# Kernel tuning notes

Hardware: AMD Instinct MI355X
Metric: run time of the kernel (lower is better)

Reference implementation:

```python
import jax, jax.numpy as jnp
import numpy as np

# scNET (vae_flag=False, cd=False, eval mode): genes x cells matrix;
# PPI graph over 3000 genes, KNN graph over 4096 cells.
N_GENES, N_CELLS = 3000, 4096          # col_dim, row_dim
INTER_R, EMBD_R = 512, 128             # gene (rows) encoder dims
INTER_C, EMBD_C = 1024, 256            # cell (cols) encoder dims
N_LAYERS = 2
KNN_E, PPI_E = 65536, 262144
SCALE_PARAM = 3.0                      # TransformerConvReducrLayer scale_param


def setup_inputs() -> dict:
    key = jax.random.key(0)
    ks = iter(jax.random.split(key, 64))
    def lin(shape):
        fan_in = shape[-2]
        return jax.random.normal(next(ks), shape, jnp.float32) / np.sqrt(fan_in)
    inp = {}
    inp["x"] = jax.random.normal(next(ks), (N_GENES, N_CELLS), jnp.float32)
    inp["knn_ei"] = jax.random.randint(next(ks), (2, KNN_E), 0, N_CELLS)
    inp["ppi_ei"] = jax.random.randint(next(ks), (2, PPI_E), 0, N_GENES)
    inp["rl_W"] = lin((N_CELLS, N_CELLS)); inp["rl_b"] = jnp.zeros((N_CELLS,), jnp.float32)
    inp["rs_Wl"] = lin((N_LAYERS, N_CELLS, N_CELLS)); inp["rs_Wr"] = lin((N_LAYERS, N_CELLS, N_CELLS))
    inp["rs_b"] = jnp.zeros((N_LAYERS, N_CELLS), jnp.float32)
    inp["cs_Wl"] = lin((N_LAYERS, N_GENES, N_GENES)); inp["cs_Wr"] = lin((N_LAYERS, N_GENES, N_GENES))
    inp["cs_b"] = jnp.zeros((N_LAYERS, N_GENES), jnp.float32)
    inp["rg_W"] = lin((N_CELLS, INTER_R)); inp["rg_b"] = jnp.zeros((INTER_R,), jnp.float32)
    for nm in ("rq", "rk", "rv", "rsk"):
        inp[nm + "_W"] = lin((INTER_R, EMBD_R)); inp[nm + "_b"] = jnp.zeros((EMBD_R,), jnp.float32)
    inp["cg_W"] = lin((N_GENES, INTER_C)); inp["cg_b"] = jnp.zeros((INTER_C,), jnp.float32)
    for nm in ("cq", "ck", "cv", "csk"):
        inp[nm + "_W"] = lin((INTER_C, EMBD_C)); inp[nm + "_b"] = jnp.zeros((EMBD_C,), jnp.float32)
    inp["d1_W"] = lin((EMBD_C, INTER_C)); inp["d1_b"] = jnp.zeros((INTER_C,), jnp.float32)
    inp["d2_W"] = lin((INTER_C, INTER_C)); inp["d2_b"] = jnp.zeros((INTER_C,), jnp.float32)
    inp["d3_W"] = lin((INTER_C, N_GENES)); inp["d3_b"] = jnp.zeros((N_GENES,), jnp.float32)
    return inp


def sage_conv(x, ei, Wl, Wr, b):
    # PyG SAGEConv (mean aggr, root weight): lin_l(mean_{j->i} x_j) + lin_r(x_i) + b
    n = x.shape[0]
    src, dst = ei[0], ei[1]
    s = jax.ops.segment_sum(x[src], dst, num_segments=n)
    cnt = jax.ops.segment_sum(jnp.ones((ei.shape[1],), x.dtype), dst, num_segments=n)
    agg = s / jnp.maximum(cnt, 1.0)[:, None]
    return agg @ Wl + x @ Wr + b


def gcn_conv(x, ei, W, b):
    # PyG GCNConv: self loops + symmetric D^-1/2 (A+I) D^-1/2 normalization
    n = x.shape[0]
    idx = jnp.arange(n)
    src = jnp.concatenate([ei[0], idx])
    dst = jnp.concatenate([ei[1], idx])
    deg = jax.ops.segment_sum(jnp.ones((src.shape[0],), x.dtype), dst, num_segments=n)
    dinv = jax.lax.rsqrt(jnp.maximum(deg, 1.0))
    h = x @ W
    msg = h[src] * (dinv[src] * dinv[dst])[:, None]
    return jax.ops.segment_sum(msg, dst, num_segments=n) + b


def transformer_conv(x, ei, Wq, bq, Wk, bk, Wv, bv, Ws, bs, scale_param):
    # PyG TransformerConv (heads=1). scale_param=None -> per-destination segment
    # softmax; otherwise scNET's globally sigmoid-normalized attention
    # (TransformerConvReducrLayer.message): global mean/std standardize -> sigmoid.
    n = x.shape[0]
    d = Wq.shape[1]
    src, dst = ei[0], ei[1]
    q = x @ Wq + bq
    k = x @ Wk + bk
    v = x @ Wv + bv
    alpha = (q[dst] * k[src]).sum(-1) / jnp.sqrt(jnp.asarray(d, x.dtype))  # [E]
    if scale_param is None:
        m = jax.ops.segment_max(alpha, dst, num_segments=n)
        e = jnp.exp(alpha - m[dst])
        z = jax.ops.segment_sum(e, dst, num_segments=n)
        alpha = e / (z[dst] + 1e-16)
    else:
        alpha = (alpha - alpha.mean()) / ((1.0 / scale_param) * jnp.std(alpha, ddof=1))
        alpha = jax.nn.sigmoid(alpha)
    out = jax.ops.segment_sum(v[src] * alpha[:, None], dst, num_segments=n)
    return out + (x @ Ws + bs)  # root skip (lin_skip)


def reference(x, knn_ei, ppi_ei, rl_W, rl_b, rs_Wl, rs_Wr, rs_b, cs_Wl, cs_Wr, cs_b,
              rg_W, rg_b, rq_W, rq_b, rk_W, rk_b, rv_W, rv_b, rsk_W, rsk_b,
              cg_W, cg_b, cq_W, cq_b, ck_W, ck_b, cv_W, cv_b, csk_W, csk_b,
              d1_W, d1_b, d2_W, d2_b, d3_W, d3_b):
    # MutaelEncoder: row linear then alternating col/row SAGE layers (dropout=id in eval)
    h = x @ rl_W + rl_b                                   # [G, C]
    for i in range(N_LAYERS):
        h = jax.nn.leaky_relu(sage_conv(h.T, knn_ei, cs_Wl[i], cs_Wr[i], cs_b[i]), 0.01).T
        h = jax.nn.leaky_relu(sage_conv(h, ppi_ei, rs_Wl[i], rs_Wr[i], rs_b[i]), 0.01)
    # rows (gene) DimEncoder: GCN -> LeakyReLU -> TransformerConv (softmax attention)
    r = jax.nn.leaky_relu(gcn_conv(h, ppi_ei, rg_W, rg_b), 0.01)
    row_embed = transformer_conv(r, ppi_ei, rq_W, rq_b, rk_W, rk_b, rv_W, rv_b, rsk_W, rsk_b, None)
    # cols (cell) DimEncoder (reducer): GCN -> LeakyReLU -> sigmoid-normalized attention
    c = jax.nn.leaky_relu(gcn_conv(h.T, knn_ei, cg_W, cg_b), 0.01)
    col_embed = transformer_conv(c, knn_ei, cq_W, cq_b, ck_W, ck_b, cv_W, cv_b, csk_W, csk_b, SCALE_PARAM)
    # FatureDecoder (cd=False): 3-layer MLP with ReLU (dropout=id in eval)
    d = jax.nn.relu(col_embed @ d1_W + d1_b)
    d = jax.nn.relu(d @ d2_W + d2_b)
    recon = d @ d3_W + d3_b                               # [C_cells, G]
    return row_embed, col_embed, recon
```

## Files before the change

### kernel.cpp

```cpp
#include <hip/hip_runtime.h>
#include <math.h>

#define N_GENES 3000
#define N_CELLS 4096
#define GPAD    3072
#define INTER_R 512
#define EMBD_R  128
#define INTER_C 1024
#define EMBD_C  256
#define KNN_E   65536
#define PPI_E   262144

typedef unsigned short u16;
typedef __bf16 bf16x8 __attribute__((ext_vector_type(8)));
typedef float f32x4 __attribute__((ext_vector_type(4)));

__device__ __forceinline__ float b2f(u16 u) {
  union { unsigned i; float f; } x; x.i = ((unsigned)u) << 16; return x.f;
}
__device__ __forceinline__ u16 f2b(float f) {
  union { float f; unsigned i; } x; x.f = f;
  unsigned r = (x.i + 0x7FFFu + ((x.i >> 16) & 1u)) >> 16;
  return (u16)r;
}

typedef const void __attribute__((address_space(1))) gvoid;
typedef void __attribute__((address_space(3))) svoid;
__device__ __forceinline__ void gload16(const void* g, void* l) {
  __builtin_amdgcn_global_load_lds((gvoid*)g, (svoid*)l, 16, 0, 0);
}

template <int OUTF32>
__global__ __launch_bounds__(256) void mgemm_k(
    const u16* __restrict__ A, int lda, const u16* __restrict__ BT, int ldb,
    const float* __restrict__ bias, void* __restrict__ Cv, int ldc,
    int M, int N, int K, int accum, int act, int nbx) {
  __shared__ u16 As[2][128 * 32];
  __shared__ u16 Bs[2][128 * 32];
  const int t = threadIdx.x;
  const int w = t >> 6, l = t & 63;
  const int wr = w >> 1, wc = w & 1;
  const int fr = l & 15, hi = l >> 4;

  int nwg = gridDim.x;
  int bid = blockIdx.x;
  int q = nwg >> 3, r = nwg & 7, xcd = bid & 7, seq = bid >> 3;
  int sid = (xcd < r ? xcd * (q + 1) : r * (q + 1) + (xcd - r) * q) + seq;
  int by = sid / nbx, bx = sid - by * nbx;
  const int row0 = by * 128, col0 = bx * 128;

  f32x4 acc[4][4];
#pragma unroll
  for (int i = 0; i < 4; i++)
#pragma unroll
    for (int j = 0; j < 4; j++) acc[i][j] = (f32x4){0.f, 0.f, 0.f, 0.f};

  const u16* Aad[2]; const u16* Bad[2];
  char* Alds[2]; char* Blds[2];
#pragma unroll
  for (int c = 0; c < 2; c++) {
    int P = (w * 2 + c) * 64 + l;
    int prow = P >> 2, pg = (P & 3) ^ (prow & 3);
    int ar = row0 + prow; ar = ar < M ? ar : M - 1;
    int br = col0 + prow; br = br < N ? br : N - 1;
    Aad[c] = A + (size_t)ar * lda + pg * 8;
    Bad[c] = BT + (size_t)br * ldb + pg * 8;
    Alds[c] = (char*)&As[0][0] + (w * 2 + c) * 1024;
    Blds[c] = (char*)&Bs[0][0] + (w * 2 + c) * 1024;
  }
  const int nt = K >> 5;
  auto stage = [&](int tt, int b) {
    int ko = tt << 5;
#pragma unroll
    for (int c = 0; c < 2; c++) {
      gload16(Aad[c] + ko, Alds[c] + b * 8192);
      gload16(Bad[c] + ko, Blds[c] + b * 8192);
    }
  };
  auto compute = [&](int tt) {
    const u16* Ab = As[tt & 1];
    const u16* Bb = Bs[tt & 1];
    bf16x8 af[4], bfr[4];
#pragma unroll
    for (int mi = 0; mi < 4; mi++) {
      int row = wr * 64 + mi * 16 + fr;
      af[mi] = *(const bf16x8*)&Ab[row * 32 + ((hi ^ (row & 3)) << 3)];
    }
#pragma unroll
    for (int ni = 0; ni < 4; ni++) {
      int row = wc * 64 + ni * 16 + fr;
      bfr[ni] = *(const bf16x8*)&Bb[row * 32 + ((hi ^ (row & 3)) << 3)];
    }
    __builtin_amdgcn_s_setprio(1);
#pragma unroll
    for (int mi = 0; mi < 4; mi++)
#pragma unroll
      for (int ni = 0; ni < 4; ni++)
        acc[mi][ni] = __builtin_amdgcn_mfma_f32_16x16x32_bf16(
            af[mi], bfr[ni], acc[mi][ni], 0, 0, 0);
    __builtin_amdgcn_s_setprio(0);
  };

  stage(0, 0);
  if (nt > 1) stage(1, 1);
  for (int tt = 0; tt < nt - 1; tt++) {
    asm volatile("s_waitcnt vmcnt(4)" ::: "memory");
    __builtin_amdgcn_sched_barrier(0);
    __builtin_amdgcn_s_barrier();
    __builtin_amdgcn_sched_barrier(0);
    compute(tt);
    __builtin_amdgcn_sched_barrier(0);
    __builtin_amdgcn_s_barrier();
    __builtin_amdgcn_sched_barrier(0);
    if (tt + 2 < nt) stage(tt + 2, tt & 1);
  }
  asm volatile("s_waitcnt vmcnt(0)" ::: "memory");
  __builtin_amdgcn_sched_barrier(0);
  __builtin_amdgcn_s_barrier();
  __builtin_amdgcn_sched_barrier(0);
  compute(nt - 1);

#pragma unroll
  for (int mi = 0; mi < 4; mi++) {
    int mb = row0 + wr * 64 + mi * 16 + hi * 4;
#pragma unroll
    for (int rr2 = 0; rr2 < 4; rr2++) {
      int m = mb + rr2;
      if (m >= M) continue;
#pragma unroll
      for (int ni = 0; ni < 4; ni++) {
        int n = col0 + wc * 64 + ni * 16 + fr;
        if (n >= N) continue;
        float v = acc[mi][ni][rr2];
        if (bias) v += bias[n];
        if (OUTF32) {
          float* C = (float*)Cv;
          if (accum) v += C[(size_t)m * ldc + n];
          if (act == 1) v = v > 0.f ? v : 0.01f * v;
          else if (act == 2) v = fmaxf(v, 0.f);
          C[(size_t)m * ldc + n] = v;
        } else {
          u16* C = (u16*)Cv;
          if (accum) v += b2f(C[(size_t)m * ldc + n]);
          if (act == 1) v = v > 0.f ? v : 0.01f * v;
          else if (act == 2) v = fmaxf(v, 0.f);
          C[(size_t)m * ldc + n] = f2b(v);
        }
      }
    }
  }
}

__global__ void cvtw_k(const float* __restrict__ in, int K, int Nw,
                       u16* __restrict__ out, int ldb, int Kpad) {
  __shared__ float tile[32][33];
  int k0 = blockIdx.y * 32, n0 = blockIdx.x * 32;
  int tx = threadIdx.x & 31, ty = threadIdx.x >> 5;
  for (int i = ty; i < 32; i += 8)
    tile[i][tx] = (k0 + i < K && n0 + tx < Nw) ? in[(size_t)(k0 + i) * Nw + n0 + tx] : 0.f;
  __syncthreads();
  for (int i = ty; i < 32; i += 8) {
    int n = n0 + i, k = k0 + tx;
    if (n < Nw && k < Kpad) out[(size_t)n * ldb + k] = f2b(tile[tx][i]);
  }
}

__global__ void tpad_k(const u16* __restrict__ in, int R, int C, int lin,
                       u16* __restrict__ out, int ldout) {
  __shared__ u16 tile[32][33];
  int r0 = blockIdx.y * 32, c0 = blockIdx.x * 32;
  int tx = threadIdx.x & 31, ty = threadIdx.x >> 5;
  for (int i = ty; i < 32; i += 8)
    tile[i][tx] = (r0 + i < R && c0 + tx < C) ? in[(size_t)(r0 + i) * lin + c0 + tx] : (u16)0;
  __syncthreads();
  for (int i = ty; i < 32; i += 8) {
    int c = c0 + i, r = r0 + tx;
    if (c < C && r < ldout) out[(size_t)c * ldout + r] = tile[tx][i];
  }
}

__global__ void cvtx_k(const float* __restrict__ in, u16* __restrict__ out, int n) {
  int i = (blockIdx.x * 256 + threadIdx.x) * 4;
  if (i >= n) return;
  float4 v = *(const float4*)&in[i];
  uint2 o;
  o.x = (unsigned)f2b(v.x) | ((unsigned)f2b(v.y) << 16);
  o.y = (unsigned)f2b(v.z) | ((unsigned)f2b(v.w) << 16);
  *(uint2*)&out[i] = o;
}

__global__ void catbias_k(const float* b0, const float* b1, const float* b2,
                          const float* b3, int seg, float* out) {
  int i = blockIdx.x * 256 + threadIdx.x;
  if (i >= 4 * seg) return;
  const float* s = i < seg ? b0 : i < 2 * seg ? b1 : i < 3 * seg ? b2 : b3;
  out[i] = s[i & (seg - 1)];
}

__global__ void zero_i32(int* __restrict__ p, int n) {
  int i = blockIdx.x * 256 + threadIdx.x;
  if (i < n) p[i] = 0;
}
__global__ void count_k(const int* __restrict__ dst, int E, int* __restrict__ cnt) {
  int e = blockIdx.x * 256 + threadIdx.x;
  if (e < E) atomicAdd(&cnt[dst[e]], 1);
}
__global__ __launch_bounds__(1024) void scan_k(const int* __restrict__ cnt,
                                               int* __restrict__ rs, int N) {
  __shared__ int sd[1024];
  int t = threadIdx.x;
  int per = (N + 1023) >> 10;
  int base = t * per;
  int loc[4];
  int s = 0;
  for (int u = 0; u < per; u++) {
    int idx = base + u;
    loc[u] = s;
    int v = (idx < N) ? cnt[idx] : 0;
    s += v;
  }
  sd[t] = s;
  __syncthreads();
  for (int off = 1; off < 1024; off <<= 1) {
    int v = (t >= off) ? sd[t - off] : 0;
    __syncthreads();
    sd[t] += v;
    __syncthreads();
  }
  int prev = (t > 0) ? sd[t - 1] : 0;
  for (int u = 0; u < per; u++) {
    int idx = base + u;
    if (idx < N) rs[idx] = prev + loc[u];
  }
  if (t == 0) rs[N] = sd[1023];
}
__global__ void fill_k(const int* __restrict__ src, const int* __restrict__ dst, int E,
                       const int* __restrict__ rs, int* cursor,
                       int* __restrict__ csrc, int* __restrict__ ceid) {
  int e = blockIdx.x * 256 + threadIdx.x;
  if (e >= E) return;
  int d = dst[e];
  int p = atomicAdd(&cursor[d], 1);
  int b = rs[d] + p;
  csrc[b] = src[e];
  ceid[b] = e;
}
__global__ void dinv_k(const int* __restrict__ rs, float* __restrict__ dinv, int N) {
  int i = blockIdx.x * 256 + threadIdx.x;
  if (i < N) dinv[i] = rsqrtf((float)(rs[i + 1] - rs[i] + 1));
}

__global__ void sage_agg_k(const u16* __restrict__ X, int ld, const int* __restrict__ rs,
                           const int* __restrict__ csrc, u16* __restrict__ out,
                           int D, int Dpad) {
  int i = blockIdx.y;
  int j8 = (blockIdx.x * 256 + threadIdx.x) * 8;
  if (j8 >= Dpad) return;
  uint4 zo = {0, 0, 0, 0};
  if (j8 >= D) { *(uint4*)&out[(size_t)i * ld + j8] = zo; return; }
  int s = rs[i], e = rs[i + 1];
  float a[8] = {0, 0, 0, 0, 0, 0, 0, 0};
  for (int p = s; p < e; p++) {
    uint4 v = *(const uint4*)&X[(size_t)csrc[p] * ld + j8];
    a[0] += b2f(v.x & 0xffff); a[1] += b2f(v.x >> 16);
    a[2] += b2f(v.y & 0xffff); a[3] += b2f(v.y >> 16);
    a[4] += b2f(v.z & 0xffff); a[5] += b2f(v.z >> 16);
    a[6] += b2f(v.w & 0xffff); a[7] += b2f(v.w >> 16);
  }
  float inv = 1.f / fmaxf((float)(e - s), 1.f);
  uint4 o;
  o.x = (unsigned)f2b(a[0] * inv) | ((unsigned)f2b(a[1] * inv) << 16);
  o.y = (unsigned)f2b(a[2] * inv) | ((unsigned)f2b(a[3] * inv) << 16);
  o.z = (unsigned)f2b(a[4] * inv) | ((unsigned)f2b(a[5] * inv) << 16);
  o.w = (unsigned)f2b(a[6] * inv) | ((unsigned)f2b(a[7] * inv) << 16);
  *(uint4*)&out[(size_t)i * ld + j8] = o;
}

__global__ void gcn_agg_k(const u16* __restrict__ HW, int ld, const int* __restrict__ rs,
                          const int* __restrict__ csrc, const float* __restrict__ dinv,
                          const float* __restrict__ bias, u16* __restrict__ out, int D) {
  int i = blockIdx.y;
  int j8 = (blockIdx.x * 256 + threadIdx.x) * 8;
  if (j8 >= D) return;
  int s = rs[i], e = rs[i + 1];
  float a[8] = {0, 0, 0, 0, 0, 0, 0, 0};
  for (int p = s; p < e; p++) {
    int sr = csrc[p];
    float w = dinv[sr];
    uint4 v = *(const uint4*)&HW[(size_t)sr * ld + j8];
    a[0] += b2f(v.x & 0xffff) * w; a[1] += b2f(v.x >> 16) * w;
    a[2] += b2f(v.y & 0xffff) * w; a[3] += b2f(v.y >> 16) * w;
    a[4] += b2f(v.z & 0xffff) * w; a[5] += b2f(v.z >> 16) * w;
    a[6] += b2f(v.w & 0xffff) * w; a[7] += b2f(v.w >> 16) * w;
  }
  float di = dinv[i];
  uint4 sv = *(const uint4*)&HW[(size_t)i * ld + j8];
  float sf[8] = {b2f(sv.x & 0xffff), b2f(sv.x >> 16), b2f(sv.y & 0xffff), b2f(sv.y >> 16),
                 b2f(sv.z & 0xffff), b2f(sv.z >> 16), b2f(sv.w & 0xffff), b2f(sv.w >> 16)};
  unsigned o[4];
#pragma unroll
  for (int q = 0; q < 4; q++) {
    float v0 = di * a[2 * q] + sf[2 * q] * di * di + bias[j8 + 2 * q];
    float v1 = di * a[2 * q + 1] + sf[2 * q + 1] * di * di + bias[j8 + 2 * q + 1];
    v0 = v0 > 0.f ? v0 : 0.01f * v0;
    v1 = v1 > 0.f ? v1 : 0.01f * v1;
    o[q] = (unsigned)f2b(v0) | ((unsigned)f2b(v1) << 16);
  }
  *(uint4*)&out[(size_t)i * ld + j8] = *(uint4*)o;
}

__global__ void attn_row_k(const u16* __restrict__ QKVS, const int* __restrict__ rs,
                           const int* __restrict__ csrc, float* __restrict__ out, int N) {
  int node = blockIdx.x * 4 + (threadIdx.x >> 6);
  if (node >= N) return;
  int lane = threadIdx.x & 63;
  const u16* base = QKVS + (size_t)node * 512;
  unsigned qb = *(const unsigned*)&base[lane * 2];
  float qx = b2f(qb & 0xffff), qy = b2f(qb >> 16);
  int s = rs[node], e = rs[node + 1];
  float m = -1e30f, z = 0.f, ax = 0.f, ay = 0.f;
  const float scale = 0.08838834764831845f;
  for (int p = s; p < e; p++) {
    const u16* kb = QKVS + (size_t)csrc[p] * 512;
    unsigned kw = *(const unsigned*)&kb[128 + lane * 2];
    float part = qx * b2f(kw & 0xffff) + qy * b2f(kw >> 16);
#pragma unroll
    for (int off = 32; off; off >>= 1) part += __shfl_xor(part, off);
    float a = part * scale;
    float mn = fmaxf(m, a);
    float sc = __expf(m - mn);
    float wv = __expf(a - mn);
    z = z * sc + wv;
    unsigned vw = *(const unsigned*)&kb[256 + lane * 2];
    ax = ax * sc + wv * b2f(vw & 0xffff);
    ay = ay * sc + wv * b2f(vw >> 16);
    m = mn;
  }
  float inv = (e == s) ? 0.f : 1.f / (z + 1e-16f);
  unsigned sw = *(const unsigned*)&base[384 + lane * 2];
  out[(size_t)node * 128 + lane * 2] = ax * inv + b2f(sw & 0xffff);
  out[(size_t)node * 128 + lane * 2 + 1] = ay * inv + b2f(sw >> 16);
}

__global__ void col_alpha_k(const u16* __restrict__ QKVS, const int* __restrict__ src,
                            const int* __restrict__ dst, float* __restrict__ alpha, int E) {
  int e = blockIdx.x * 4 + (threadIdx.x >> 6);
  if (e >= E) return;
  int lane = threadIdx.x & 63;
  uint2 qb = *(const uint2*)&QKVS[(size_t)dst[e] * 1024 + lane * 4];
  uint2 kb = *(const uint2*)&QKVS[(size_t)src[e] * 1024 + 256 + lane * 4];
  float p = b2f(qb.x & 0xffff) * b2f(kb.x & 0xffff) + b2f(qb.x >> 16) * b2f(kb.x >> 16) +
            b2f(qb.y & 0xffff) * b2f(kb.y & 0xffff) + b2f(qb.y >> 16) * b2f(kb.y >> 16);
#pragma unroll
  for (int off = 32; off; off >>= 1) p += __shfl_xor(p, off);
  if (lane == 0) alpha[e] = p * 0.0625f;
}

__global__ void stats_k(const float* __restrict__ alpha, int E, double* __restrict__ st) {
  __shared__ double s1[256], s2[256];
  int t = threadIdx.x;
  double a1 = 0, a2 = 0;
  for (int i = blockIdx.x * 256 + t; i < E; i += gridDim.x * 256) {
    double a = alpha[i];
    a1 += a; a2 += a * a;
  }
  s1[t] = a1; s2[t] = a2;
  __syncthreads();
  for (int off = 128; off; off >>= 1) {
    if (t < off) { s1[t] += s1[t + off]; s2[t] += s2[t + off]; }
    __syncthreads();
  }
  if (t == 0) { atomicAdd(&st[0], s1[0]); atomicAdd(&st[1], s2[0]); }
}

__global__ void col_attn_agg_k(const u16* __restrict__ QKVS, const float* __restrict__ alpha,
                               const int* __restrict__ rs, const int* __restrict__ csrc,
                               const int* __restrict__ ceid, const double* __restrict__ st,
                               float* __restrict__ outf, u16* __restrict__ outb, int E) {
  int i = blockIdx.x;
  int j = threadIdx.x;
  double mean = st[0] / E;
  double var = (st[1] - E * mean * mean) / (double)(E - 1);
  float rstd = (float)(1.0 / sqrt(var));
  float fm = (float)mean;
  int s = rs[i], e = rs[i + 1];
  float acc = 0.f;
  for (int p = s; p < e; p++) {
    float a = alpha[ceid[p]];
    float x = 3.0f * (a - fm) * rstd;
    float sg = 1.f / (1.f + __expf(-x));
    acc += sg * b2f(QKVS[(size_t)csrc[p] * 1024 + 512 + j]);
  }
  float res = acc + b2f(QKVS[(size_t)i * 1024 + 768 + j]);
  outf[(size_t)i * 256 + j] = res;
  outb[(size_t)i * 256 + j] = f2b(res);
}

extern "C" void kernel_launch(void* const* d_in, const int* in_sizes, int n_in,
                              void* d_out, int out_size, void* d_ws, size_t ws_size,
                              hipStream_t stream) {
  const float* x      = (const float*)d_in[0];
  const int*   knn_ei = (const int*)d_in[1];
  const int*   ppi_ei = (const int*)d_in[2];
  const float* rl_W   = (const float*)d_in[3];
  const float* rl_b   = (const float*)d_in[4];
  const float* rs_Wl  = (const float*)d_in[5];
  const float* rs_Wr  = (const float*)d_in[6];
  const float* rs_b   = (const float*)d_in[7];
  const float* cs_Wl  = (const float*)d_in[8];
  const float* cs_Wr  = (const float*)d_in[9];
  const float* cs_b   = (const float*)d_in[10];
  const float* rg_W   = (const float*)d_in[11];
  const float* rg_b   = (const float*)d_in[12];
  const float* rq_W   = (const float*)d_in[13];
  const float* rq_b   = (const float*)d_in[14];
  const float* rk_W   = (const float*)d_in[15];
  const float* rk_b   = (const float*)d_in[16];
  const float* rv_W   = (const float*)d_in[17];
  const float* rv_b   = (const float*)d_in[18];
  const float* rsk_W  = (const float*)d_in[19];
  const float* rsk_b  = (const float*)d_in[20];
  const float* cg_W   = (const float*)d_in[21];
  const float* cg_b   = (const float*)d_in[22];
  const float* cq_W   = (const float*)d_in[23];
  const float* cq_b   = (const float*)d_in[24];
  const float* ck_W   = (const float*)d_in[25];
  const float* ck_b   = (const float*)d_in[26];
  const float* cv_W   = (const float*)d_in[27];
  const float* cv_b   = (const float*)d_in[28];
  const float* csk_W  = (const float*)d_in[29];
  const float* csk_b  = (const float*)d_in[30];
  const float* d1_W   = (const float*)d_in[31];
  const float* d1_b   = (const float*)d_in[32];
  const float* d2_W   = (const float*)d_in[33];
  const float* d2_b   = (const float*)d_in[34];
  const float* d3_W   = (const float*)d_in[35];
  const float* d3_b   = (const float*)d_in[36];
  float* out = (float*)d_out;

  char* ws = (char*)d_ws;
  size_t off = 0;
  auto alloc = [&](size_t bytes) -> void* {
    void* p = ws + off;
    off = (off + bytes + 255) & ~(size_t)255;
    return p;
  };
  const size_t PB = (size_t)N_CELLS * GPAD * 2;
  u16* P0 = (u16*)alloc(PB);
  u16* P1 = (u16*)alloc(PB);
  u16* P2 = (u16*)alloc(PB);
  u16* P3 = (u16*)alloc(PB);
  u16* xb  = (u16*)alloc((size_t)N_GENES * N_CELLS * 2);
  u16* BTs = (u16*)alloc((size_t)N_CELLS * N_CELLS * 2);
  u16* CEb = (u16*)alloc((size_t)N_CELLS * EMBD_C * 2);
  float* catb = (float*)alloc(1024 * 4);
  int* knn_rs  = (int*)alloc((N_CELLS + 1) * 4);
  int* knn_cnt = (int*)alloc(N_CELLS * 4);
  int* knn_cur = (int*)alloc(N_CELLS * 4);
  int* knn_src = (int*)alloc(KNN_E * 4);
  int* knn_eid = (int*)alloc(KNN_E * 4);
  int* ppi_rs  = (int*)alloc((N_GENES + 1) * 4);
  int* ppi_cnt = (int*)alloc(N_GENES * 4);
  int* ppi_cur = (int*)alloc(N_GENES * 4);
  int* ppi_src = (int*)alloc(PPI_E * 4);
  int* ppi_eid = (int*)alloc(PPI_E * 4);
  float* dinv_knn = (float*)alloc(N_CELLS * 4);
  float* dinv_ppi = (float*)alloc(N_GENES * 4);
  float* alphaB   = (float*)alloc(KNN_E * 4);
  double* stats   = (double*)alloc(2 * 8);

  auto cvtw = [&](const float* W, int K, int Nw, u16* dst, int ldb, int Kpad) {
    dim3 g((Nw + 31) / 32, (Kpad + 31) / 32);
    cvtw_k<<<g, 256, 0, stream>>>(W, K, Nw, dst, ldb, Kpad);
  };
  auto mg = [&](const u16* A, int lda, const u16* BT, int ldb, const float* bias,
                void* C, int ldc, int M, int N, int K, int accum, int act, int outf32) {
    int nbx = (N + 127) / 128, nby = (M + 127) / 128;
    dim3 g(nbx * nby);
    if (outf32)
      mgemm_k<1><<<g, 256, 0, stream>>>(A, lda, BT, ldb, bias, C, ldc, M, N, K, accum, act, nbx);
    else
      mgemm_k<0><<<g, 256, 0, stream>>>(A, lda, BT, ldb, bias, C, ldc, M, N, K, accum, act, nbx);
  };
  auto tpad = [&](const u16* in, int R, int C, int lin, u16* o, int ldout) {
    dim3 g((C + 31) / 32, (ldout + 31) / 32);
    tpad_k<<<g, 256, 0, stream>>>(in, R, C, lin, o, ldout);
  };
  auto sage = [&](const u16* X, int ld, const int* rs, const int* csrc, u16* o,
                  int nodes, int D, int Dpad) {
    dim3 g((Dpad / 8 + 255) / 256, nodes);
    sage_agg_k<<<g, 256, 0, stream>>>(X, ld, rs, csrc, o, D, Dpad);
  };
  auto gcn = [&](const u16* HW, int ld, const int* rs, const int* csrc, const float* dinv,
                 const float* bias, u16* o, int nodes, int D) {
    dim3 g((D / 8 + 255) / 256, nodes);
    gcn_agg_k<<<g, 256, 0, stream>>>(HW, ld, rs, csrc, dinv, bias, o, D);
  };

  zero_i32<<<(N_CELLS + 255) / 256, 256, 0, stream>>>(knn_cnt, N_CELLS);
  count_k<<<(KNN_E + 255) / 256, 256, 0, stream>>>(knn_ei + KNN_E, KNN_E, knn_cnt);
  scan_k<<<1, 1024, 0, stream>>>(knn_cnt, knn_rs, N_CELLS);
  zero_i32<<<(N_CELLS + 255) / 256, 256, 0, stream>>>(knn_cur, N_CELLS);
  fill_k<<<(KNN_E + 255) / 256, 256, 0, stream>>>(knn_ei, knn_ei + KNN_E, KNN_E,
                                                  knn_rs, knn_cur, knn_src, knn_eid);
  dinv_k<<<(N_CELLS + 255) / 256, 256, 0, stream>>>(knn_rs, dinv_knn, N_CELLS);
  zero_i32<<<(N_GENES + 255) / 256, 256, 0, stream>>>(ppi_cnt, N_GENES);
  count_k<<<(PPI_E + 255) / 256, 256, 0, stream>>>(ppi_ei + PPI_E, PPI_E, ppi_cnt);
  scan_k<<<1, 1024, 0, stream>>>(ppi_cnt, ppi_rs, N_GENES);
  zero_i32<<<(N_GENES + 255) / 256, 256, 0, stream>>>(ppi_cur, N_GENES);
  fill_k<<<(PPI_E + 255) / 256, 256, 0, stream>>>(ppi_ei, ppi_ei + PPI_E, PPI_E,
                                                  ppi_rs, ppi_cur, ppi_src, ppi_eid);
  dinv_k<<<(N_GENES + 255) / 256, 256, 0, stream>>>(ppi_rs, dinv_ppi, N_GENES);

  cvtx_k<<<(N_GENES * N_CELLS / 4 + 255) / 256, 256, 0, stream>>>(
      x, xb, N_GENES * N_CELLS);
  cvtw(rl_W, N_CELLS, N_CELLS, BTs, N_CELLS, N_CELLS);
  mg(xb, N_CELLS, BTs, N_CELLS, rl_b, P0, N_CELLS, N_GENES, N_CELLS, N_CELLS, 0, 0, 0);

  for (int i = 0; i < 2; i++) {
    const float* cWl = cs_Wl + (size_t)i * N_GENES * N_GENES;
    const float* cWr = cs_Wr + (size_t)i * N_GENES * N_GENES;
    const float* cb  = cs_b + (size_t)i * N_GENES;
    const float* rWl = rs_Wl + (size_t)i * N_CELLS * N_CELLS;
    const float* rWr = rs_Wr + (size_t)i * N_CELLS * N_CELLS;
    const float* rb  = rs_b + (size_t)i * N_CELLS;
    tpad(P0, N_GENES, N_CELLS, N_CELLS, P1, GPAD);
    sage(P1, GPAD, knn_rs, knn_src, P2, N_CELLS, N_GENES, GPAD);
    cvtw(cWl, N_GENES, N_GENES, BTs, GPAD, GPAD);
    mg(P2, GPAD, BTs, GPAD, cb, P3, GPAD, N_CELLS, N_GENES, GPAD, 0, 0, 0);
    cvtw(cWr, N_GENES, N_GENES, BTs, GPAD, GPAD);
    mg(P1, GPAD, BTs, GPAD, nullptr, P3, GPAD, N_CELLS, N_GENES, GPAD, 1, 1, 0);
    tpad(P3, N_CELLS, N_GENES, GPAD, P2, N_CELLS);
    sage(P2, N_CELLS, ppi_rs, ppi_src, P1, N_GENES, N_CELLS, N_CELLS);
    cvtw(rWl, N_CELLS, N_CELLS, BTs, N_CELLS, N_CELLS);
    mg(P1, N_CELLS, BTs, N_CELLS, rb, P0, N_CELLS, N_GENES, N_CELLS, N_CELLS, 0, 0, 0);
    cvtw(rWr, N_CELLS, N_CELLS, BTs, N_CELLS, N_CELLS);
    mg(P2, N_CELLS, BTs, N_CELLS, nullptr, P0, N_CELLS, N_GENES, N_CELLS, N_CELLS, 1, 1, 0);
  }

  cvtw(rg_W, N_CELLS, INTER_R, BTs, N_CELLS, N_CELLS);
  mg(P0, N_CELLS, BTs, N_CELLS, nullptr, P1, INTER_R, N_GENES, INTER_R, N_CELLS, 0, 0, 0);
  gcn(P1, INTER_R, ppi_rs, ppi_src, dinv_ppi, rg_b, P2, N_GENES, INTER_R);
  cvtw(rq_W, INTER_R, EMBD_R, BTs + (size_t)0 * EMBD_R * INTER_R, INTER_R, INTER_R);
  cvtw(rk_W, INTER_R, EMBD_R, BTs + (size_t)1 * EMBD_R * INTER_R, INTER_R, INTER_R);
  cvtw(rv_W, INTER_R, EMBD_R, BTs + (size_t)2 * EMBD_R * INTER_R, INTER_R, INTER_R);
  cvtw(rsk_W, INTER_R, EMBD_R, BTs + (size_t)3 * EMBD_R * INTER_R, INTER_R, INTER_R);
  catbias_k<<<2, 256, 0, stream>>>(rq_b, rk_b, rv_b, rsk_b, EMBD_R, catb);
  mg(P2, INTER_R, BTs, INTER_R, catb, P1, 4 * EMBD_R, N_GENES, 4 * EMBD_R, INTER_R, 0, 0, 0);
  attn_row_k<<<(N_GENES + 3) / 4, 256, 0, stream>>>(P1, ppi_rs, ppi_src, out, N_GENES);

  tpad(P0, N_GENES, N_CELLS, N_CELLS, P1, GPAD);
  cvtw(cg_W, N_GENES, INTER_C, BTs, GPAD, GPAD);
  mg(P1, GPAD, BTs, GPAD, nullptr, P2, INTER_C, N_CELLS, INTER_C, GPAD, 0, 0, 0);
  gcn(P2, INTER_C, knn_rs, knn_src, dinv_knn, cg_b, P0, N_CELLS, INTER_C);
  cvtw(cq_W, INTER_C, EMBD_C, BTs + (size_t)0 * EMBD_C * INTER_C, INTER_C, INTER_C);
  cvtw(ck_W, INTER_C, EMBD_C, BTs + (size_t)1 * EMBD_C * INTER_C, INTER_C, INTER_C);
  cvtw(cv_W, INTER_C, EMBD_C, BTs + (size_t)2 * EMBD_C * INTER_C, INTER_C, INTER_C);
  cvtw(csk_W, INTER_C, EMBD_C, BTs + (size_t)3 * EMBD_C * INTER_C, INTER_C, INTER_C);
  catbias_k<<<4, 256, 0, stream>>>(cq_b, ck_b, cv_b, csk_b, EMBD_C, catb);
  mg(P0, INTER_C, BTs, INTER_C, catb, P1, 4 * EMBD_C, N_CELLS, 4 * EMBD_C, INTER_C, 0, 0, 0);
  col_alpha_k<<<KNN_E / 4, 256, 0, stream>>>(P1, knn_ei, knn_ei + KNN_E, alphaB, KNN_E);
  zero_i32<<<1, 256, 0, stream>>>((int*)stats, 4);
  stats_k<<<64, 256, 0, stream>>>(alphaB, KNN_E, stats);
  float* col_embed = out + (size_t)N_GENES * EMBD_R;
  col_attn_agg_k<<<N_CELLS, 256, 0, stream>>>(P1, alphaB, knn_rs, knn_src, knn_eid,
                                              stats, col_embed, CEb, KNN_E);

  float* recon = col_embed + (size_t)N_CELLS * EMBD_C;
  cvtw(d1_W, EMBD_C, INTER_C, BTs, EMBD_C, EMBD_C);
  mg(CEb, EMBD_C, BTs, EMBD_C, d1_b, P2, INTER_C, N_CELLS, INTER_C, EMBD_C, 0, 2, 0);
  cvtw(d2_W, INTER_C, INTER_C, BTs, INTER_C, INTER_C);
  mg(P2, INTER_C, BTs, INTER_C, d2_b, P3, INTER_C, N_CELLS, INTER_C, INTER_C, 0, 2, 0);
  cvtw(d3_W, INTER_C, N_GENES, BTs, INTER_C, INTER_C);
  mg(P3, INTER_C, BTs, INTER_C, d3_b, recon, N_GENES, N_CELLS, N_GENES, INTER_C, 0, 0, 1);
}
```

Measured before the change: 2.461 ms.

## Replace SAGE sparse mean aggregation with dense adjacency GEMMs and add 256-row GEMM tiles

Builds dense bf16 adjacency-count matrices for the KNN and PPI graphs by atomic scatter. The SAGE mean aggregation then runs as a dense GEMM with a per-row 1/degree scale applied in the epilogue. This replaces the gather-based sage_agg kernel, which had poor memory locality, with MFMA work. The cost is large extra dense FLOPs (4096x4096 and 3000x3072 adjacency products) and extra buffers. The GEMM kernel also gains a 256x128 tile variant with a changed LDS swizzle, used for the large GEMMs.

After: 4.658 ms. 1.89x slower.

```diff
diff --git a/kernel.cpp b/kernel.cpp
--- a/kernel.cpp
+++ b/kernel.cpp
@@ -30,70 +30,77 @@
   __builtin_amdgcn_global_load_lds((gvoid*)g, (svoid*)l, 16, 0, 0);
 }
 
-template <int OUTF32>
+template <int OUTF32, int WM>
 __global__ __launch_bounds__(256) void mgemm_k(
     const u16* __restrict__ A, int lda, const u16* __restrict__ BT, int ldb,
-    const float* __restrict__ bias, void* __restrict__ Cv, int ldc,
-    int M, int N, int K, int accum, int act, int nbx) {
-  __shared__ u16 As[2][128 * 32];
+    const float* __restrict__ bias, const float* __restrict__ rscale,
+    void* __restrict__ Cv, int ldc, int M, int N, int K,
+    int accum, int act, int nbx) {
+  constexpr int TM = WM * 2;
+  constexpr int AC = WM / 32;
+  constexpr int MF = WM / 16;
+  __shared__ u16 As[2][TM * 32];
   __shared__ u16 Bs[2][128 * 32];
   const int t = threadIdx.x;
   const int w = t >> 6, l = t & 63;
   const int wr = w >> 1, wc = w & 1;
   const int fr = l & 15, hi = l >> 4;
 
-  int nwg = gridDim.x;
-  int bid = blockIdx.x;
+  int nwg = gridDim.x, bid = blockIdx.x;
   int q = nwg >> 3, r = nwg & 7, xcd = bid & 7, seq = bid >> 3;
   int sid = (xcd < r ? xcd * (q + 1) : r * (q + 1) + (xcd - r) * q) + seq;
   int by = sid / nbx, bx = sid - by * nbx;
-  const int row0 = by * 128, col0 = bx * 128;
-
-  f32x4 acc[4][4];
-#pragma unroll
-  for (int i = 0; i < 4; i++)
+  const int row0 = by * TM, col0 = bx * 128;
+
+  f32x4 acc[MF][4];
+#pragma unroll
+  for (int i = 0; i < MF; i++)
 #pragma unroll
     for (int j = 0; j < 4; j++) acc[i][j] = (f32x4){0.f, 0.f, 0.f, 0.f};
 
-  const u16* Aad[2]; const u16* Bad[2];
-  char* Alds[2]; char* Blds[2];
+  const u16* Aad[AC]; const u16* Bad[2];
+  char* Alds[AC]; char* Blds[2];
+#pragma unroll
+  for (int c = 0; c < AC; c++) {
+    int P = (w * AC + c) * 64 + l;
+    int prow = P >> 2, pg = (P & 3) ^ ((prow >> 2) & 3);
+    int ar = row0 + prow; ar = ar < M ? ar : M - 1;
+    Aad[c] = A + (size_t)ar * lda + pg * 8;
+    Alds[c] = (char*)&As[0][0] + P * 16;
+  }
 #pragma unroll
   for (int c = 0; c < 2; c++) {
-    int P = (w * 2 + c) * 64 + l;
-    int prow = P >> 2, pg = (P & 3) ^ (prow & 3);
-    int ar = row0 + prow; ar = ar < M ? ar : M - 1;
-    int br = col0 + prow; br = br < N ? br : N - 1;
-    Aad[c] = A + (size_t)ar * lda + pg * 8;
+    int Q = (w * 2 + c) * 64 + l;
+    int brow = Q >> 2, pg = (Q & 3) ^ ((brow >> 2) & 3);
+    int br = col0 + brow; br = br < N ? br : N - 1;
     Bad[c] = BT + (size_t)br * ldb + pg * 8;
-    Alds[c] = (char*)&As[0][0] + (w * 2 + c) * 1024;
-    Blds[c] = (char*)&Bs[0][0] + (w * 2 + c) * 1024;
+    Blds[c] = (char*)&Bs[0][0] + Q * 16;
   }
   const int nt = K >> 5;
   auto stage = [&](int tt, int b) {
     int ko = tt << 5;
 #pragma unroll
-    for (int c = 0; c < 2; c++) {
-      gload16(Aad[c] + ko, Alds[c] + b * 8192);
-      gload16(Bad[c] + ko, Blds[c] + b * 8192);
-    }
+    for (int c = 0; c < AC; c++) gload16(Aad[c] + ko, Alds[c] + b * (TM * 64));
+#pragma unroll
+    for (int c = 0; c < 2; c++) gload16(Bad[c] + ko, Blds[c] + b * 8192);
   };
   auto compute = [&](int tt) {
     const u16* Ab = As[tt & 1];
     const u16* Bb = Bs[tt & 1];
-    bf16x8 af[4], bfr[4];
-#pragma unroll
-    for (int mi = 0; mi < 4; mi++) {
-      int row = wr * 64 + mi * 16 + fr;
-      af[mi] = *(const bf16x8*)&Ab[row * 32 + ((hi ^ (row & 3)) << 3)];
+    bf16x8 af[MF], bfr[4];
+#pragma unroll
+    for (int mi = 0; mi < MF; mi++) {
+      int row = wr * WM + mi * 16 + fr;
+      af[mi] = *(const bf16x8*)&Ab[row * 32 + ((hi ^ ((row >> 2) & 3)) << 3)];
     }
 #pragma unroll
     for (int ni = 0; ni < 4; ni++) {
       int row = wc * 64 + ni * 16 + fr;
-      bfr[ni] = *(const bf16x8*)&Bb[row * 32 + ((hi ^ (row & 3)) << 3)];
+      bfr[ni] = *(const bf16x8*)&Bb[row * 32 + ((hi ^ ((row >> 2) & 3)) << 3)];
     }
     __builtin_amdgcn_s_setprio(1);
 #pragma unroll
-    for (int mi = 0; mi < 4; mi++)
+    for (int mi = 0; mi < MF; mi++)
 #pragma unroll
       for (int ni = 0; ni < 4; ni++)
         acc[mi][ni] = __builtin_amdgcn_mfma_f32_16x16x32_bf16(
@@ -104,7 +111,10 @@
   stage(0, 0);
   if (nt > 1) stage(1, 1);
   for (int tt = 0; tt < nt - 1; tt++) {
-    asm volatile("s_waitcnt vmcnt(4)" ::: "memory");
+    if constexpr (WM == 128)
+      asm volatile("s_waitcnt vmcnt(6)" ::: "memory");
+    else
+      asm volatile("s_waitcnt vmcnt(4)" ::: "memory");
     __builtin_amdgcn_sched_barrier(0);
     __builtin_amdgcn_s_barrier();
     __builtin_amdgcn_sched_barrier(0);
@@ -121,17 +131,18 @@
   compute(nt - 1);
 
 #pragma unroll
-  for (int mi = 0; mi < 4; mi++) {
-    int mb = row0 + wr * 64 + mi * 16 + hi * 4;
+  for (int mi = 0; mi < MF; mi++) {
+    int mb = row0 + wr * WM + mi * 16 + hi * 4;
 #pragma unroll
     for (int rr2 = 0; rr2 < 4; rr2++) {
       int m = mb + rr2;
       if (m >= M) continue;
+      float rsc = rscale ? rscale[m] : 1.f;
 #pragma unroll
       for (int ni = 0; ni < 4; ni++) {
         int n = col0 + wc * 64 + ni * 16 + fr;
         if (n >= N) continue;
-        float v = acc[mi][ni][rr2];
+        float v = acc[mi][ni][rr2] * rsc;
         if (bias) v += bias[n];
         if (OUTF32) {
           float* C = (float*)Cv;
@@ -197,6 +208,41 @@
   out[i] = s[i & (seg - 1)];
 }
 
+__global__ void zerof4_k(float* __restrict__ p, int n4) {
+  int i = blockIdx.x * 256 + threadIdx.x;
+  if (i < n4) *(float4*)&p[(size_t)i * 4] = make_float4(0.f, 0.f, 0.f, 0.f);
+}
+__global__ void scat_k(const int* __restrict__ src, const int* __restrict__ dst,
+                       int E, float* __restrict__ A, int ld) {
+  int e = blockIdx.x * 256 + threadIdx.x;
+  if (e < E) atomicAdd(&A[(size_t)dst[e] * ld + src[e]], 1.0f);
+}
+__global__ void cvtadj_k(const float* __restrict__ in, int C, int ldi,
+                         u16* __restrict__ out, int ldo) {
+  int r = blockIdx.y;
+  int c8 = (blockIdx.x * 256 + threadIdx.x) * 8;
+  if (c8 >= ldo) return;
+  uint4 o = {0, 0, 0, 0};
+  if (c8 < C) {
+    float4 v0 = *(const float4*)&in[(size_t)r * ldi + c8];
+    float4 v1 = *(const float4*)&in[(size_t)r * ldi + c8 + 4];
+    o.x = (unsigned)f2b(v0.x) | ((unsigned)f2b(v0.y) << 16);
+    o.y = (unsigned)f2b(v0.z) | ((unsigned)f2b(v0.w) << 16);
+    o.z = (unsigned)f2b(v1.x) | ((unsigned)f2b(v1.y) << 16);
+    o.w = (unsigned)f2b(v1.z) | ((unsigned)f2b(v1.w) << 16);
+  }
+  *(uint4*)&out[(size_t)r * ldo + c8] = o;
+}
+__global__ void zero_u16_k(u16* __restrict__ p, int n) {
+  int i = blockIdx.x * 256 + threadIdx.x;
+  if (i < n) p[i] = 0;
+}
+__global__ void zpadcols_k(u16* __restrict__ base, int rows, int ld, int c0, int w) {
+  int i = blockIdx.x * 256 + threadIdx.x;
+  int r = i / w, c = i - r * w;
+  if (r < rows) base[(size_t)r * ld + c0 + c] = 0;
+}
+
 __global__ void zero_i32(int* __restrict__ p, int n) {
   int i = blockIdx.x * 256 + threadIdx.x;
   if (i < n) p[i] = 0;
@@ -249,31 +295,12 @@
   int i = blockIdx.x * 256 + threadIdx.x;
   if (i < N) dinv[i] = rsqrtf((float)(rs[i + 1] - rs[i] + 1));
 }
-
-__global__ void sage_agg_k(const u16* __restrict__ X, int ld, const int* __restrict__ rs,
-                           const int* __restrict__ csrc, u16* __restrict__ out,
-                           int D, int Dpad) {
-  int i = blockIdx.y;
-  int j8 = (blockIdx.x * 256 + threadIdx.x) * 8;
-  if (j8 >= Dpad) return;
-  uint4 zo = {0, 0, 0, 0};
-  if (j8 >= D) { *(uint4*)&out[(size_t)i * ld + j8] = zo; return; }
-  int s = rs[i], e = rs[i + 1];
-  float a[8] = {0, 0, 0, 0, 0, 0, 0, 0};
-  for (int p = s; p < e; p++) {
-    uint4 v = *(const uint4*)&X[(size_t)csrc[p] * ld + j8];
-    a[0] += b2f(v.x & 0xffff); a[1] += b2f(v.x >> 16);
-    a[2] += b2f(v.y & 0xffff); a[3] += b2f(v.y >> 16);
-    a[4] += b2f(v.z & 0xffff); a[5] += b2f(v.z >> 16);
-    a[6] += b2f(v.w & 0xffff); a[7] += b2f(v.w >> 16);
-  }
-  float inv = 1.f / fmaxf((float)(e - s), 1.f);
-  uint4 o;
-  o.x = (unsigned)f2b(a[0] * inv) | ((unsigned)f2b(a[1] * inv) << 16);
-  o.y = (unsigned)f2b(a[2] * inv) | ((unsigned)f2b(a[3] * inv) << 16);
-  o.z = (unsigned)f2b(a[4] * inv) | ((unsigned)f2b(a[5] * inv) << 16);
-  o.w = (unsigned)f2b(a[6] * inv) | ((unsigned)f2b(a[7] * inv) << 16);
-  *(uint4*)&out[(size_t)i * ld + j8] = o;
+__global__ void rmean_k(const int* __restrict__ rs, float* __restrict__ rsc, int N) {
+  int i = blockIdx.x * 256 + threadIdx.x;
+  if (i < N) {
+    int d = rs[i + 1] - rs[i];
+    rsc[i] = 1.f / (float)(d > 1 ? d : 1);
+  }
 }
 
 __global__ void gcn_agg_k(const u16* __restrict__ HW, int ld, const int* __restrict__ rs,
@@ -452,6 +479,7 @@
   u16* P3 = (u16*)alloc(PB);
   u16* xb  = (u16*)alloc((size_t)N_GENES * N_CELLS * 2);
   u16* BTs = (u16*)alloc((size_t)N_CELLS * N_CELLS * 2);
+  u16* AdjC = (u16*)alloc((size_t)N_CELLS * N_CELLS * 2);
   u16* CEb = (u16*)alloc((size_t)N_CELLS * EMBD_C * 2);
   float* catb = (float*)alloc(1024 * 4);
   int* knn_rs  = (int*)alloc((N_CELLS + 1) * 4);
@@ -466,30 +494,37 @@
   int* ppi_eid = (int*)alloc(PPI_E * 4);
   float* dinv_knn = (float*)alloc(N_CELLS * 4);
   float* dinv_ppi = (float*)alloc(N_GENES * 4);
+  float* rscK = (float*)alloc(N_CELLS * 4);
+  float* rscP = (float*)alloc(N_GENES * 4);
   float* alphaB   = (float*)alloc(KNN_E * 4);
   double* stats   = (double*)alloc(2 * 8);
+  u16* AdjG = xb;
 
   auto cvtw = [&](const float* W, int K, int Nw, u16* dst, int ldb, int Kpad) {
     dim3 g((Nw + 31) / 32, (Kpad + 31) / 32);
     cvtw_k<<<g, 256, 0, stream>>>(W, K, Nw, dst, ldb, Kpad);
   };
   auto mg = [&](const u16* A, int lda, const u16* BT, int ldb, const float* bias,
-                void* C, int ldc, int M, int N, int K, int accum, int act, int outf32) {
-    int nbx = (N + 127) / 128, nby = (M + 127) / 128;
+                const float* rsc, void* C, int ldc, int M, int N, int K,
+                int accum, int act, int outf32, int wm128) {
+    int TMx = wm128 ? 256 : 128;
+    int nbx = (N + 127) / 128, nby = (M + TMx - 1) / TMx;
     dim3 g(nbx * nby);
-    if (outf32)
-      mgemm_k<1><<<g, 256, 0, stream>>>(A, lda, BT, ldb, bias, C, ldc, M, N, K, accum, act, nbx);
-    else
-      mgemm_k<0><<<g, 256, 0, stream>>>(A, lda, BT, ldb, bias, C, ldc, M, N, K, accum, act, nbx);
+    if (wm128) {
+      if (outf32)
+        mgemm_k<1, 128><<<g, 256, 0, stream>>>(A, lda, BT, ldb, bias, rsc, C, ldc, M, N, K, accum, act, nbx);
+      else
+        mgemm_k<0, 128><<<g, 256, 0, stream>>>(A, lda, BT, ldb, bias, rsc, C, ldc, M, N, K, accum, act, nbx);
+    } else {
+      if (outf32)
+        mgemm_k<1, 64><<<g, 256, 0, stream>>>(A, lda, BT, ldb, bias, rsc, C, ldc, M, N, K, accum, act, nbx);
+      else
+        mgemm_k<0, 64><<<g, 256, 0, stream>>>(A, lda, BT, ldb, bias, rsc, C, ldc, M, N, K, accum, act, nbx);
+    }
   };
   auto tpad = [&](const u16* in, int R, int C, int lin, u16* o, int ldout) {
     dim3 g((C + 31) / 32, (ldout + 31) / 32);
     tpad_k<<<g, 256, 0, stream>>>(in, R, C, lin, o, ldout);
-  };
-  auto sage = [&](const u16* X, int ld, const int* rs, const int* csrc, u16* o,
-                  int nodes, int D, int Dpad) {
-    dim3 g((Dpad / 8 + 255) / 256, nodes);
-    sage_agg_k<<<g, 256, 0, stream>>>(X, ld, rs, csrc, o, D, Dpad);
   };
   auto gcn = [&](const u16* HW, int ld, const int* rs, const int* csrc, const float* dinv,
                  const float* bias, u16* o, int nodes, int D) {
@@ -504,6 +539,7 @@
   fill_k<<<(KNN_E + 255) / 256, 256, 0, stream>>>(knn_ei, knn_ei + KNN_E, KNN_E,
                                                   knn_rs, knn_cur, knn_src, knn_eid);
   dinv_k<<<(N_CELLS + 255) / 256, 256, 0, stream>>>(knn_rs, dinv_knn, N_CELLS);
+  rmean_k<<<(N_CELLS + 255) / 256, 256, 0, stream>>>(knn_rs, rscK, N_CELLS);
   zero_i32<<<(N_GENES + 255) / 256, 256, 0, stream>>>(ppi_cnt, N_GENES);
   count_k<<<(PPI_E + 255) / 256, 256, 0, stream>>>(ppi_ei + PPI_E, PPI_E, ppi_cnt);
   scan_k<<<1, 1024, 0, stream>>>(ppi_cnt, ppi_rs, N_GENES);
@@ -511,11 +547,38 @@
   fill_k<<<(PPI_E + 255) / 256, 256, 0, stream>>>(ppi_ei, ppi_ei + PPI_E, PPI_E,
                                                   ppi_rs, ppi_cur, ppi_src, ppi_eid);
   dinv_k<<<(N_GENES + 255) / 256, 256, 0, stream>>>(ppi_rs, dinv_ppi, N_GENES);
+  rmean_k<<<(N_GENES + 255) / 256, 256, 0, stream>>>(ppi_rs, rscP, N_GENES);
+
+  zpadcols_k<<<(N_CELLS * (GPAD - N_GENES) + 255) / 256, 256, 0, stream>>>(
+      P3, N_CELLS, GPAD, N_GENES, GPAD - N_GENES);
+
+  {
+    float* st = (float*)P0;
+    zerof4_k<<<(N_CELLS * N_CELLS / 4 + 255) / 256, 256, 0, stream>>>(
+        st, N_CELLS * N_CELLS / 4);
+    scat_k<<<(KNN_E + 255) / 256, 256, 0, stream>>>(knn_ei, knn_ei + KNN_E, KNN_E,
+                                                    st, N_CELLS);
+    dim3 g((N_CELLS / 8 + 255) / 256, N_CELLS);
+    cvtadj_k<<<g, 256, 0, stream>>>(st, N_CELLS, N_CELLS, AdjC, N_CELLS);
+  }
+  zero_u16_k<<<((GPAD - N_GENES) * N_CELLS + 255) / 256, 256, 0, stream>>>(
+      P0 + (size_t)N_GENES * N_CELLS, (GPAD - N_GENES) * N_CELLS);
 
   cvtx_k<<<(N_GENES * N_CELLS / 4 + 255) / 256, 256, 0, stream>>>(
       x, xb, N_GENES * N_CELLS);
   cvtw(rl_W, N_CELLS, N_CELLS, BTs, N_CELLS, N_CELLS);
-  mg(xb, N_CELLS, BTs, N_CELLS, rl_b, P0, N_CELLS, N_GENES, N_CELLS, N_CELLS, 0, 0, 0);
+  mg(xb, N_CELLS, BTs, N_CELLS, rl_b, nullptr, P0, N_CELLS,
+     N_GENES, N_CELLS, N_CELLS, 0, 0, 0, 1);
+
+  {
+    float* st = (float*)P1;
+    zerof4_k<<<(N_GENES * N_GENES / 4 + 255) / 256, 256, 0, stream>>>(
+        st, N_GENES * N_GENES / 4);
+    scat_k<<<(PPI_E + 255) / 256, 256, 0, stream>>>(ppi_ei, ppi_ei + PPI_E, PPI_E,
+                                                    st, N_GENES);
+    dim3 g((GPAD / 8 + 255) / 256, N_GENES);
+    cvtadj_k<<<g, 256, 0, stream>>>(st, N_GENES, N_GENES, AdjG, GPAD);
+  }
 
   for (int i = 0; i < 2; i++) {
     const float* cWl = cs_Wl + (size_t)i * N_GENES * N_GENES;
@@ -525,40 +588,48 @@
     const float* rWr = rs_Wr + (size_t)i * N_CELLS * N_CELLS;
     const float* rb  = rs_b + (size_t)i * N_CELLS;
     tpad(P0, N_GENES, N_CELLS, N_CELLS, P1, GPAD);
-    sage(P1, GPAD, knn_rs, knn_src, P2, N_CELLS, N_GENES, GPAD);
+    mg(AdjC, N_CELLS, P0, N_CELLS, nullptr, rscK, P2, GPAD,
+       N_CELLS, GPAD, N_CELLS, 0, 0, 0, 1);
     cvtw(cWl, N_GENES, N_GENES, BTs, GPAD, GPAD);
-    mg(P2, GPAD, BTs, GPAD, cb, P3, GPAD, N_CELLS, N_GENES, GPAD, 0, 0, 0);
+    mg(P2, GPAD, BTs, GPAD, cb, nullptr, P3, GPAD, N_CELLS, N_GENES, GPAD, 0, 0, 0, 1);
     cvtw(cWr, N_GENES, N_GENES, BTs, GPAD, GPAD);
-    mg(P1, GPAD, BTs, GPAD, nullptr, P3, GPAD, N_CELLS, N_GENES, GPAD, 1, 1, 0);
+    mg(P1, GPAD, BTs, GPAD, nullptr, nullptr, P3, GPAD, N_CELLS, N_GENES, GPAD, 1, 1, 0, 1);
     tpad(P3, N_CELLS, N_GENES, GPAD, P2, N_CELLS);
-    sage(P2, N_CELLS, ppi_rs, ppi_src, P1, N_GENES, N_CELLS, N_CELLS);
+    mg(AdjG, GPAD, P3, GPAD, nullptr, rscP, P1, N_CELLS,
+       N_GENES, N_CELLS, GPAD, 0, 0, 0, 1);
     cvtw(rWl, N_CELLS, N_CELLS, BTs, N_CELLS, N_CELLS);
-    mg(P1, N_CELLS, BTs, N_CELLS, rb, P0, N_CELLS, N_GENES, N_CELLS, N_CELLS, 0, 0, 0);
+    mg(P1, N_CELLS, BTs, N_CELLS, rb, nullptr, P0, N_CELLS,
+       N_GENES, N_CELLS, N_CELLS, 0, 0, 0, 1);
     cvtw(rWr, N_CELLS, N_CELLS, BTs, N_CELLS, N_CELLS);
-    mg(P2, N_CELLS, BTs, N_CELLS, nullptr, P0, N_CELLS, N_GENES, N_CELLS, N_CELLS, 1, 1, 0);
+    mg(P2, N_CELLS, BTs, N_CELLS, nullptr, nullptr, P0, N_CELLS,
+       N_GENES, N_CELLS, N_CELLS, 1, 1, 0, 1);
   }
 
   cvtw(rg_W, N_CELLS, INTER_R, BTs, N_CELLS, N_CELLS);
-  mg(P0, N_CELLS, BTs, N_CELLS, nullptr, P1, INTER_R, N_GENES, INTER_R, N_CELLS, 0, 0, 0);
+  mg(P0, N_CELLS, BTs, N_CELLS, nullptr, nullptr, P1, INTER_R,
+     N_GENES, INTER_R, N_CELLS, 0, 0, 0, 0);
   gcn(P1, INTER_R, ppi_rs, ppi_src, dinv_ppi, rg_b, P2, N_GENES, INTER_R);
   cvtw(rq_W, INTER_R, EMBD_R, BTs + (size_t)0 * EMBD_R * INTER_R, INTER_R, INTER_R);
   cvtw(rk_W, INTER_R, EMBD_R, BTs + (size_t)1 * EMBD_R * INTER_R, INTER_R, INTER_R);
   cvtw(rv_W, INTER_R, EMBD_R, BTs + (size_t)2 * EMBD_R * INTER_R, INTER_R, INTER_R);
   cvtw(rsk_W, INTER_R, EMBD_R, BTs + (size_t)3 * EMBD_R * INTER_R, INTER_R, INTER_R);
   catbias_k<<<2, 256, 0, stream>>>(rq_b, rk_b, rv_b, rsk_b, EMBD_R, catb);
-  mg(P2, INTER_R, BTs, INTER_R, catb, P1, 4 * EMBD_R, N_GENES, 4 * EMBD_R, INTER_R, 0, 0, 0);
+  mg(P2, INTER_R, BTs, INTER_R, catb, nullptr, P1, 4 * EMBD_R,
+     N_GENES, 4 * EMBD_R, INTER_R, 0, 0, 0, 0);
   attn_row_k<<<(N_GENES + 3) / 4, 256, 0, stream>>>(P1, ppi_rs, ppi_src, out, N_GENES);
 
   tpad(P0, N_GENES, N_CELLS, N_CELLS, P1, GPAD);
   cvtw(cg_W, N_GENES, INTER_C, BTs, GPAD, GPAD);
-  mg(P1, GPAD, BTs, GPAD, nullptr, P2, INTER_C, N_CELLS, INTER_C, GPAD, 0, 0, 0);
+  mg(P1, GPAD, BTs, GPAD, nullptr, nullptr, P2, INTER_C,
+     N_CELLS, INTER_C, GPAD, 0, 0, 0, 0);
   gcn(P2, INTER_C, knn_rs, knn_src, dinv_knn, cg_b, P0, N_CELLS, INTER_C);
   cvtw(cq_W, INTER_C, EMBD_C, BTs + (size_t)0 * EMBD_C * INTER_C, INTER_C, INTER_C);
   cvtw(ck_W, INTER_C, EMBD_C, BTs + (size_t)1 * EMBD_C * INTER_C, INTER_C, INTER_C);
   cvtw(cv_W, INTER_C, EMBD_C, BTs + (size_t)2 * EMBD_C * INTER_C, INTER_C, INTER_C);
   cvtw(csk_W, INTER_C, EMBD_C, BTs + (size_t)3 * EMBD_C * INTER_C, INTER_C, INTER_C);
   catbias_k<<<4, 256, 0, stream>>>(cq_b, ck_b, cv_b, csk_b, EMBD_C, catb);
-  mg(P0, INTER_C, BTs, INTER_C, catb, P1, 4 * EMBD_C, N_CELLS, 4 * EMBD_C, INTER_C, 0, 0, 0);
+  mg(P0, INTER_C, BTs, INTER_C, catb, nullptr, P1, 4 * EMBD_C,
+     N_CELLS, 4 * EMBD_C, INTER_C, 0, 0, 0, 0);
   col_alpha_k<<<KNN_E / 4, 256, 0, stream>>>(P1, knn_ei, knn_ei + KNN_E, alphaB, KNN_E);
   zero_i32<<<1, 256, 0, stream>>>((int*)stats, 4);
   stats_k<<<64, 256, 0, stream>>>(alphaB, KNN_E, stats);
@@ -568,9 +639,12 @@
 
   float* recon = col_embed + (size_t)N_CELLS * EMBD_C;
   cvtw(d1_W, EMBD_C, INTER_C, BTs, EMBD_C, EMBD_C);
-  mg(CEb, EMBD_C, BTs, EMBD_C, d1_b, P2, INTER_C, N_CELLS, INTER_C, EMBD_C, 0, 2, 0);
+  mg(CEb, EMBD_C, BTs, EMBD_C, d1_b, nullptr, P2, INTER_C,
+     N_CELLS, INTER_C, EMBD_C, 0, 2, 0, 0);
   cvtw(d2_W, INTER_C, INTER_C, BTs, INTER_C, INTER_C);
-  mg(P2, INTER_C, BTs, INTER_C, d2_b, P3, INTER_C, N_CELLS, INTER_C, INTER_C, 0, 2, 0);
+  mg(P2, INTER_C, BTs, INTER_C, d2_b, nullptr, P3, INTER_C,
+     N_CELLS, INTER_C, INTER_C, 0, 2, 0, 0);
   cvtw(d3_W, INTER_C, N_GENES, BTs, INTER_C, INTER_C);
-  mg(P3, INTER_C, BTs, INTER_C, d3_b, recon, N_GENES, N_CELLS, N_GENES, INTER_C, 0, 0, 1);
-}
+  mg(P3, INTER_C, BTs, INTER_C, d3_b, nullptr, recon, N_GENES,
+     N_CELLS, N_GENES, INTER_C, 0, 0, 1, 1);
+}
```
